# Optimization experiments

Measured on AMD Instinct MI355X. Metric: run time of the kernel, lower is better.

Reference implementation:

```python
import jax, jax.numpy as jnp
import numpy as np

N = 50000      # nodes
E = 800000     # edges (avg in-degree ~16)
IN = 64        # in_size
OUT = 64       # out_size
DELTA = 2.83   # PNA delta ~ log(avg_degree + 1)
MOM_EPS = 1e-30
BN_EPS = 1e-5


def setup_inputs() -> dict:
    key = jax.random.key(0)
    ks = jax.random.split(key, 8)
    node_feat = jax.random.normal(ks[0], (N, IN), dtype=jnp.float32)
    # Linear M: (2*IN -> IN); store weight as (2*IN, IN) for x @ W
    Wm = jax.random.normal(ks[1], (2 * IN, IN), dtype=jnp.float32) * (1.0 / np.sqrt(2 * IN))
    bm = jnp.zeros((IN,), jnp.float32)
    # Linear U: ((4 aggs * 3 scalers + 1) * IN -> OUT) = (13*IN -> OUT)
    Wu = jax.random.normal(ks[2], (13 * IN, OUT), dtype=jnp.float32) * (1.0 / np.sqrt(13 * IN))
    bu = jnp.zeros((OUT,), jnp.float32)
    gamma = jnp.ones((OUT,), jnp.float32)
    beta = jnp.zeros((OUT,), jnp.float32)
    src = jax.random.randint(ks[3], (E,), 0, N, dtype=jnp.int32)
    dst = jax.random.randint(ks[4], (E,), 0, N, dtype=jnp.int32)
    return {"node_feat": node_feat, "Wm": Wm, "bm": bm, "Wu": Wu, "bu": bu,
            "gamma": gamma, "beta": beta, "src": src, "dst": dst}


def _pna_forward(node_feat, Wm, bm, Wu, bu, gamma, beta, src, dst):
    # message MLP: M(h_src || h_dst) computed without materializing the concat
    msg = node_feat[src] @ Wm[:IN] + node_feat[dst] @ Wm[IN:] + bm  # (E, IN)

    deg = jax.ops.segment_sum(jnp.ones((E,), msg.dtype), dst, num_segments=N)  # (N,)
    safe_deg = jnp.maximum(deg, 1.0)[:, None]
    has_nbr = (deg > 0.0)[:, None]

    # multi-statistic ragged segment reduce
    s = jax.ops.segment_sum(msg, dst, num_segments=N)
    mean = s / safe_deg
    mean_sq = jax.ops.segment_sum(msg * msg, dst, num_segments=N) / safe_deg
    var = jax.nn.relu(mean_sq - mean * mean)
    std = jnp.sqrt(var + MOM_EPS)
    mx = jnp.where(has_nbr, jax.ops.segment_max(msg, dst, num_segments=N), 0.0)
    mn = jnp.where(has_nbr, jax.ops.segment_min(msg, dst, num_segments=N), 0.0)

    h = jnp.concatenate([mean, mx, mn, std], axis=1)  # (N, 4*IN)

    # scalers: identity, amplification log(D+1)/delta, attenuation delta/log(D+1)
    logD = jnp.log(deg + 1.0)[:, None]
    safe_logD = jnp.where(logD > 0.0, logD, 1.0)  # zero-degree rows masked below
    h_all = jnp.concatenate([h, h * (safe_logD / DELTA), h * (DELTA / safe_logD)], axis=1)
    h_neigh = jnp.where(has_nbr, h_all, 0.0)  # zero-degree nodes get 0 (DGL behavior)

    # update MLP + graph size norm (single graph: snorm = 1/sqrt(N))
    z = jnp.concatenate([node_feat, h_neigh], axis=1) @ Wu + bu  # (N, OUT)
    snorm = 1.0 / jnp.sqrt(jnp.asarray(N, z.dtype))
    z = z * snorm

    # BatchNorm1d, training mode (batch stats, biased variance)
    mu = jnp.mean(z, axis=0)
    v = jnp.mean((z - mu) ** 2, axis=0)
    return (z - mu) / jnp.sqrt(v + BN_EPS) * gamma + beta


def reference(node_feat, Wm, bm, Wu, bu, gamma, beta, src, dst):
    return _pna_forward(node_feat, Wm, bm, Wu, bu, gamma, beta, src, dst)
```

## Files before the change

### kernel.cpp

```cpp
#include <hip/hip_runtime.h>
#include <hip/hip_bf16.h>


#define DELTA_C 2.83f
#define BN_EPS_C 1e-5f
#define MOM_EPS_C 1e-30f
#define FLT_BIG 3.402823466e38f
#define BSHIFT 7
#define NBMAX 512

typedef __attribute__((ext_vector_type(8))) short bf16x8;
typedef __attribute__((ext_vector_type(4))) float f32x4;

static __device__ __forceinline__ unsigned short f2bf(float f) {
    unsigned u = __float_as_uint(f);
    unsigned r = (u + 0x7FFFu + ((u >> 16) & 1u)) >> 16;
    return (unsigned short)r;
}
static __device__ __forceinline__ unsigned pack2(float a, float b) {
    return (unsigned)f2bf(a) | ((unsigned)f2bf(b) << 16);
}
static __device__ __forceinline__ float bflo(unsigned u) { return __uint_as_float(u << 16); }
static __device__ __forceinline__ float bfhi(unsigned u) { return __uint_as_float(u & 0xFFFF0000u); }

__global__ __launch_bounds__(256) void repack_wu(
    const float* __restrict__ Wu, short* __restrict__ Wup,
    int* __restrict__ bcnt, int* __restrict__ gcur, float* __restrict__ bnacc)
{
    int t = threadIdx.x;
    if (blockIdx.x == 0) {
        bcnt[t] = 0; bcnt[t + 256] = 0;
        gcur[t] = 0; gcur[t + 256] = 0;
        if (t < 128) bnacc[t] = 0.f;
    }
    int idx = blockIdx.x * 256 + t;
    int lane = idx & 63, c = (idx >> 6) & 3, kc = idx >> 8;
    int kbase = kc * 32 + (lane >> 4) * 8;
    int col = c * 16 + (lane & 15);
    unsigned short o[8];
    #pragma unroll
    for (int i = 0; i < 8; ++i)
        o[i] = f2bf(Wu[(size_t)(kbase + i) * 64 + col]);
    uint4 u;
    u.x = o[0] | ((unsigned)o[1] << 16);
    u.y = o[2] | ((unsigned)o[3] << 16);
    u.z = o[4] | ((unsigned)o[5] << 16);
    u.w = o[6] | ((unsigned)o[7] << 16);
    *(uint4*)(Wup + (size_t)idx * 8) = u;
}

__global__ __launch_bounds__(256) void proj_ab(
    const float* __restrict__ x, const float* __restrict__ Wm,
    unsigned* __restrict__ Ab, float* __restrict__ B,
    unsigned* __restrict__ xbu, int n,
    const int* __restrict__ dst, int* __restrict__ bcnt, int e, int nb_chunk)
{
    __shared__ float wm[128][68];
    __shared__ float xs[64][68];
    __shared__ int h[NBMAX];
    int t = threadIdx.x;
    for (int i = t; i < 2048; i += 256) {
        int k = i >> 4, c4 = (i & 15) << 2;
        *(float4*)&wm[k][c4] = *(const float4*)&Wm[k * 64 + c4];
    }
    int row0 = blockIdx.x * 64;
    for (int i = t; i < 1024; i += 256) {
        int r = i >> 4, k4 = (i & 15) << 2;
        int row = row0 + r;
        float4 v = make_float4(0.f, 0.f, 0.f, 0.f);
        if (row < n) v = *(const float4*)&x[(size_t)row * 64 + k4];
        *(float4*)&xs[r][k4] = v;
    }
    __syncthreads();
    int tr = t >> 4, tc = t & 15, c0 = tc << 2;
    float a[4][4] = {}; float b[4][4] = {};
    #pragma unroll 8
    for (int k = 0; k < 64; ++k) {
        float4 wa = *(float4*)&wm[k][c0];
        float4 wb = *(float4*)&wm[64 + k][c0];
        #pragma unroll
        for (int i = 0; i < 4; ++i) {
            float xv = xs[tr * 4 + i][k];
            a[i][0] += xv * wa.x; a[i][1] += xv * wa.y; a[i][2] += xv * wa.z; a[i][3] += xv * wa.w;
            b[i][0] += xv * wb.x; b[i][1] += xv * wb.y; b[i][2] += xv * wb.z; b[i][3] += xv * wb.w;
        }
    }
    #pragma unroll
    for (int i = 0; i < 4; ++i) {
        int r = tr * 4 + i;
        int row = row0 + r;
        uint2 xp;
        xp.x = pack2(xs[r][c0], xs[r][c0 + 1]);
        xp.y = pack2(xs[r][c0 + 2], xs[r][c0 + 3]);
        *(uint2*)&xbu[(size_t)row * 32 + (c0 >> 1)] = xp;
        if (row < n) {
            uint2 ap;
            ap.x = pack2(a[i][0], a[i][1]);
            ap.y = pack2(a[i][2], a[i][3]);
            *(uint2*)&Ab[(size_t)row * 32 + (c0 >> 1)] = ap;
            *(float4*)&B[(size_t)row * 64 + c0] = make_float4(b[i][0], b[i][1], b[i][2], b[i][3]);
        }
    }
    if (blockIdx.x < nb_chunk) {
        __syncthreads();
        for (int bb = t; bb < NBMAX; bb += 256) h[bb] = 0;
        __syncthreads();
        int base = blockIdx.x * 4096;
        int cnt = min(4096, e - base);
        for (int i = t; i < cnt; i += 256)
            atomicAdd(&h[dst[base + i] >> BSHIFT], 1);
        __syncthreads();
        for (int bb = t; bb < NBMAX; bb += 256)
            if (h[bb]) atomicAdd(&bcnt[bb], h[bb]);
    }
}

__global__ __launch_bounds__(256) void bin_scatter(
    const int* __restrict__ src, const int* __restrict__ dst,
    const int* __restrict__ bcnt, int* __restrict__ gcur,
    unsigned* __restrict__ pairs_out, int e)
{
    __shared__ int hcnt[NBMAX], hstart[NBMAX], hcur[NBMAX], gpos[NBMAX], sgoff[NBMAX];
    __shared__ unsigned pairs[4096];
    int t = threadIdx.x;
    int base = blockIdx.x * 4096;
    int cnt = min(4096, e - base);
    for (int b = t; b < NBMAX; b += 256) hcnt[b] = 0;
    if (t < 64) {
        int v0 = bcnt[t * 8],     v1 = bcnt[t * 8 + 1], v2 = bcnt[t * 8 + 2], v3 = bcnt[t * 8 + 3];
        int v4 = bcnt[t * 8 + 4], v5 = bcnt[t * 8 + 5], v6 = bcnt[t * 8 + 6], v7 = bcnt[t * 8 + 7];
        int s = v0 + v1 + v2 + v3 + v4 + v5 + v6 + v7;
        int inc = s;
        #pragma unroll
        for (int st = 1; st < 64; st <<= 1) {
            int u = __shfl_up(inc, st);
            if (t >= st) inc += u;
        }
        int ex = inc - s;
        sgoff[t * 8] = ex;         ex += v0;
        sgoff[t * 8 + 1] = ex;     ex += v1;
        sgoff[t * 8 + 2] = ex;     ex += v2;
        sgoff[t * 8 + 3] = ex;     ex += v3;
        sgoff[t * 8 + 4] = ex;     ex += v4;
        sgoff[t * 8 + 5] = ex;     ex += v5;
        sgoff[t * 8 + 6] = ex;     ex += v6;
        sgoff[t * 8 + 7] = ex;
    }
    __syncthreads();

    int ls[16], ld[16];
    #pragma unroll
    for (int j = 0; j < 16; ++j) {
        int i = t + j * 256;
        ls[j] = 0; ld[j] = -1;
        if (i < cnt) {
            ls[j] = src[base + i];
            ld[j] = dst[base + i];
            atomicAdd(&hcnt[ld[j] >> BSHIFT], 1);
        }
    }
    __syncthreads();
    if (t < 64) {
        int v[8]; int s = 0;
        #pragma unroll
        for (int j = 0; j < 8; ++j) { v[j] = hcnt[t * 8 + j]; s += v[j]; }
        int inc = s;
        #pragma unroll
        for (int st = 1; st < 64; st <<= 1) {
            int u = __shfl_up(inc, st);
            if (t >= st) inc += u;
        }
        int ex = inc - s;
        #pragma unroll
        for (int j = 0; j < 8; ++j) {
            hstart[t * 8 + j] = ex;
            hcur[t * 8 + j] = ex;
            ex += v[j];
        }
    }
    __syncthreads();
    #pragma unroll
    for (int j = 0; j < 16; ++j) {
        if (ld[j] >= 0) {
            int pos = atomicAdd(&hcur[ld[j] >> BSHIFT], 1);
            pairs[pos] = ((unsigned)ls[j] << 16) | (unsigned)ld[j];
        }
    }
    __syncthreads();
    for (int b = t; b < NBMAX; b += 256) {
        int c = hcnt[b];
        if (c) gpos[b] = sgoff[b] + atomicAdd(&gcur[b], c);
    }
    __syncthreads();
    #pragma unroll
    for (int j = 0; j < 16; ++j) {
        int i = t + j * 256;
        if (i < cnt) {
            unsigned p = pairs[i];
            int b = (int)(p & 0xFFFFu) >> BSHIFT;
            pairs_out[gpos[b] + (i - hstart[b])] = p;
        }
    }
}

__global__ __launch_bounds__(128) void csr_fill(
    const unsigned* __restrict__ pairs, const int* __restrict__ bcnt,
    int* __restrict__ offs, int* __restrict__ csr, int n, int e)
{
    __shared__ int hist[128], pref[128], cur[128], sbase[1];
    int b = blockIdx.x, t = threadIdx.x;
    if (t < 64) {
        int acc = 0;
        for (int k = t; k < b; k += 64) acc += bcnt[k];
        acc += __shfl_down(acc, 32); acc += __shfl_down(acc, 16);
        acc += __shfl_down(acc, 8);  acc += __shfl_down(acc, 4);
        acc += __shfl_down(acc, 2);  acc += __shfl_down(acc, 1);
        if (t == 0) sbase[0] = acc;
    }
    hist[t] = 0;
    __syncthreads();
    int base = sbase[0], cnt = bcnt[b];
    int node0 = b << BSHIFT;
    for (int i = t; i < cnt; i += 128)
        atomicAdd(&hist[pairs[base + i] & 127u], 1);
    __syncthreads();
    if (t < 64) {
        int v0 = hist[2 * t], v1 = hist[2 * t + 1];
        int s = v0 + v1, inc = s;
        #pragma unroll
        for (int st = 1; st < 64; st <<= 1) {
            int u = __shfl_up(inc, st);
            if (t >= st) inc += u;
        }
        int ex = inc - s;
        pref[2 * t] = ex;       cur[2 * t] = ex;
        pref[2 * t + 1] = ex + v0; cur[2 * t + 1] = ex + v0;
    }
    __syncthreads();
    int node = node0 + t;
    if (node < n) offs[node] = base + pref[t];
    if (b == gridDim.x - 1 && t == 0) offs[n] = e;
    for (int i = t; i < cnt; i += 128) {
        unsigned p = pairs[base + i];
        int pos = atomicAdd(&cur[p & 127u], 1);
        csr[base + pos] = (int)(p >> 16);
    }
}

__global__ __launch_bounds__(256) void node_reduce(
    const unsigned* __restrict__ Ab, const float* __restrict__ Bp,
    const float* __restrict__ bm,
    const int* __restrict__ offs, const int* __restrict__ csr,
    unsigned* __restrict__ hbu, float* __restrict__ s1, float* __restrict__ s2,
    int n, int npad)
{
    int wid = threadIdx.x >> 6;
    int lane = threadIdx.x & 63;
    int node = blockIdx.x * 4 + wid;
    if (node >= npad) return;
    unsigned* hrow = hbu + (size_t)node * 128;
    int l32 = lane & 31;
    int half = lane >> 5;
    int beg = 0, dg = 0;
    if (node < n) { beg = offs[node]; dg = offs[node + 1] - beg; }
    if (dg == 0) {
        if (half == 0) {
            hrow[l32] = 0u; hrow[32 + l32] = 0u; hrow[64 + l32] = 0u; hrow[96 + l32] = 0u;
        }
        if (lane == 0) { s1[node] = 0.f; s2[node] = 0.f; }
        return;
    }

    float s0 = 0.f, s1a = 0.f, ss0 = 0.f, ss1 = 0.f;
    float mx0 = -FLT_BIG, mx1 = -FLT_BIG, mn0 = FLT_BIG, mn1 = FLT_BIG;

#define ACC(u) { float v0 = bflo(u), v1 = bfhi(u);                          \
    s0 += v0; s1a += v1;                                                    \
    ss0 = fmaf(v0, v0, ss0); ss1 = fmaf(v1, v1, ss1);                       \
    mx0 = fmaxf(mx0, v0); mx1 = fmaxf(mx1, v1);                             \
    mn0 = fminf(mn0, v0); mn1 = fminf(mn1, v1); }
#define GA(sel) Ab[(size_t)(sel) * 32 + l32]

    int j = beg, end = beg + dg;
    for (; j + 15 < end; j += 16) {
        int i0 = csr[j],      i1 = csr[j + 1],  i2 = csr[j + 2],  i3 = csr[j + 3];
        int i4 = csr[j + 4],  i5 = csr[j + 5],  i6 = csr[j + 6],  i7 = csr[j + 7];
        int i8 = csr[j + 8],  i9 = csr[j + 9],  i10 = csr[j + 10], i11 = csr[j + 11];
        int i12 = csr[j + 12], i13 = csr[j + 13], i14 = csr[j + 14], i15 = csr[j + 15];
        unsigned u0 = GA(half ? i1 : i0);
        unsigned u1 = GA(half ? i3 : i2);
        unsigned u2 = GA(half ? i5 : i4);
        unsigned u3 = GA(half ? i7 : i6);
        unsigned u4 = GA(half ? i9 : i8);
        unsigned u5 = GA(half ? i11 : i10);
        unsigned u6 = GA(half ? i13 : i12);
        unsigned u7 = GA(half ? i15 : i14);
        ACC(u0); ACC(u1); ACC(u2); ACC(u3);
        ACC(u4); ACC(u5); ACC(u6); ACC(u7);
    }
    for (; j + 7 < end; j += 8) {
        int i0 = csr[j],     i1 = csr[j + 1], i2 = csr[j + 2], i3 = csr[j + 3];
        int i4 = csr[j + 4], i5 = csr[j + 5], i6 = csr[j + 6], i7 = csr[j + 7];
        unsigned u0 = GA(half ? i1 : i0);
        unsigned u1 = GA(half ? i3 : i2);
        unsigned u2 = GA(half ? i5 : i4);
        unsigned u3 = GA(half ? i7 : i6);
        ACC(u0); ACC(u1); ACC(u2); ACC(u3);
    }
    for (; j + 1 < end; j += 2) {
        int i0 = csr[j], i1 = csr[j + 1];
        unsigned u0 = GA(half ? i1 : i0);
        ACC(u0);
    }
    if (j < end) {
        unsigned u0 = GA(csr[j]);
        if (half == 0) ACC(u0);
    }
#undef GA
#undef ACC

    s0 += __shfl_xor(s0, 32);  s1a += __shfl_xor(s1a, 32);
    ss0 += __shfl_xor(ss0, 32); ss1 += __shfl_xor(ss1, 32);
    mx0 = fmaxf(mx0, __shfl_xor(mx0, 32)); mx1 = fmaxf(mx1, __shfl_xor(mx1, 32));
    mn0 = fminf(mn0, __shfl_xor(mn0, 32)); mn1 = fminf(mn1, __shfl_xor(mn1, 32));

    float fd = (float)dg, inv = 1.0f / fd;
    float2 bv = *(const float2*)(Bp + (size_t)node * 64 + 2 * l32);
    float2 bmv = *(const float2*)(bm + 2 * l32);
    float bn0 = bv.x + bmv.x, bn1 = bv.y + bmv.y;
    float ma0 = s0 * inv, ma1 = s1a * inv;
    float var0 = ss0 * inv - ma0 * ma0; if (var0 < 0.f) var0 = 0.f;
    float var1 = ss1 * inv - ma1 * ma1; if (var1 < 0.f) var1 = 0.f;
    float sd0 = sqrtf(var0 + MOM_EPS_C), sd1 = sqrtf(var1 + MOM_EPS_C);

    if (half == 0) {
        hrow[l32]      = pack2(ma0 + bn0, ma1 + bn1);
        hrow[32 + l32] = pack2(mx0 + bn0, mx1 + bn1);
        hrow[64 + l32] = pack2(mn0 + bn0, mn1 + bn1);
        hrow[96 + l32] = pack2(sd0, sd1);
    }
    if (lane == 0) {
        float logD = logf(fd + 1.0f);
        s1[node] = logD / DELTA_C;
        s2[node] = DELTA_C / logD;
    }
}

__global__ __launch_bounds__(256) void gemm_mfma(
    const short* __restrict__ xb, const short* __restrict__ hb,
    const float* __restrict__ s1p, const float* __restrict__ s2p,
    const short* __restrict__ Wup, const float* __restrict__ bu,
    float* __restrict__ z, float* __restrict__ bnacc, int n, float snorm)
{
    __shared__ float bnl[4][2][64];
    int t = threadIdx.x;
    int lane = t & 63, w = t >> 6;
    int rb = blockIdx.x * 128 + w * 32;
    int r16 = lane & 15, kg = lane >> 4;

    f32x4 accx[2][4] = {};
    f32x4 acc1[2][4] = {};
    f32x4 acc2[2][4] = {};
    f32x4 acc3[2][4] = {};

    const short* xr0 = xb + (size_t)(rb + r16) * 64 + kg * 8;
    const short* xr1 = xr0 + 16 * 64;

    #pragma unroll
    for (int kc = 0; kc < 2; ++kc) {
        bf16x8 a0 = *(const bf16x8*)(xr0 + kc * 32);
        bf16x8 a1 = *(const bf16x8*)(xr1 + kc * 32);
        #pragma unroll
        for (int c = 0; c < 4; ++c) {
            bf16x8 b = *(const bf16x8*)(Wup + (size_t)((kc * 4 + c) * 64 + lane) * 8);
            accx[0][c] = __builtin_amdgcn_mfma_f32_16x16x32_bf16(a0, b, accx[0][c], 0, 0, 0);
            accx[1][c] = __builtin_amdgcn_mfma_f32_16x16x32_bf16(a1, b, accx[1][c], 0, 0, 0);
        }
    }

    const short* hr0 = hb + (size_t)(rb + r16) * 256 + kg * 8;
    const short* hr1 = hr0 + 16 * 256;

    #pragma unroll 1
    for (int kh = 0; kh < 8; ++kh) {
        bf16x8 a0 = *(const bf16x8*)(hr0 + kh * 32);
        bf16x8 a1 = *(const bf16x8*)(hr1 + kh * 32);
        #pragma unroll
        for (int c = 0; c < 4; ++c) {
            bf16x8 b1 = *(const bf16x8*)(Wup + (size_t)(((2  + kh) * 4 + c) * 64 + lane) * 8);
            bf16x8 b2 = *(const bf16x8*)(Wup + (size_t)(((10 + kh) * 4 + c) * 64 + lane) * 8);
            bf16x8 b3 = *(const bf16x8*)(Wup + (size_t)(((18 + kh) * 4 + c) * 64 + lane) * 8);
            acc1[0][c] = __builtin_amdgcn_mfma_f32_16x16x32_bf16(a0, b1, acc1[0][c], 0, 0, 0);
            acc1[1][c] = __builtin_amdgcn_mfma_f32_16x16x32_bf16(a1, b1, acc1[1][c], 0, 0, 0);
            acc2[0][c] = __builtin_amdgcn_mfma_f32_16x16x32_bf16(a0, b2, acc2[0][c], 0, 0, 0);
            acc2[1][c] = __builtin_amdgcn_mfma_f32_16x16x32_bf16(a1, b2, acc2[1][c], 0, 0, 0);
            acc3[0][c] = __builtin_amdgcn_mfma_f32_16x16x32_bf16(a0, b3, acc3[0][c], 0, 0, 0);
            acc3[1][c] = __builtin_amdgcn_mfma_f32_16x16x32_bf16(a1, b3, acc3[1][c], 0, 0, 0);
        }
    }

    float cs[4] = {}, css[4] = {};
    #pragma unroll
    for (int s = 0; s < 2; ++s) {
        int r0 = rb + s * 16 + kg * 4;
        float s1v[4], s2v[4];
        #pragma unroll
        for (int r = 0; r < 4; ++r) { s1v[r] = s1p[r0 + r]; s2v[r] = s2p[r0 + r]; }
        #pragma unroll
        for (int c = 0; c < 4; ++c) {
            int col = c * 16 + r16;
            float bval = bu[col];
            #pragma unroll
            for (int r = 0; r < 4; ++r) {
                int row = r0 + r;
                if (row < n) {
                    float v = (accx[s][c][r] + acc1[s][c][r]
                            + s1v[r] * acc2[s][c][r] + s2v[r] * acc3[s][c][r] + bval) * snorm;
                    z[(size_t)row * 64 + col] = v;
                    cs[c] += v;
                    css[c] = fmaf(v, v, css[c]);
                }
            }
        }
    }
    #pragma unroll
    for (int c = 0; c < 4; ++c) {
        float a = cs[c];  a += __shfl_xor(a, 16); a += __shfl_xor(a, 32); cs[c] = a;
        float b = css[c]; b += __shfl_xor(b, 16); b += __shfl_xor(b, 32); css[c] = b;
    }
    if (lane < 16) {
        #pragma unroll
        for (int c = 0; c < 4; ++c) {
            bnl[w][0][c * 16 + lane] = cs[c];
            bnl[w][1][c * 16 + lane] = css[c];
        }
    }
    __syncthreads();
    if (t < 128) {
        int st = t >> 6, cc = t & 63;
        float tot = bnl[0][st][cc] + bnl[1][st][cc] + bnl[2][st][cc] + bnl[3][st][cc];
        atomicAdd(&bnacc[st * 64 + cc], tot);
    }
}

__global__ __launch_bounds__(256) void bn_apply(
    float* __restrict__ z, const float* __restrict__ acc,
    const float* __restrict__ gamma, const float* __restrict__ beta, int n)
{
    float inv_n = 1.0f / (float)n;
    int tid = blockIdx.x * 256 + threadIdx.x;
    int c0 = (tid * 4) & 63;
    float sc[4], sh[4];
    #pragma unroll
    for (int k = 0; k < 4; ++k) {
        int c = c0 + k;
        float mu = acc[c] * inv_n;
        float var = acc[64 + c] * inv_n - mu * mu;
        if (var < 0.f) var = 0.f;
        float inv = rsqrtf(var + BN_EPS_C) * gamma[c];
        sc[k] = inv;
        sh[k] = beta[c] - mu * inv;
    }
    int total4 = n * 16;
    int stride = gridDim.x * 256;
    for (int i = tid; i < total4; i += stride) {
        float4 v = *(float4*)&z[(size_t)i * 4];
        v.x = fmaf(v.x, sc[0], sh[0]);
        v.y = fmaf(v.y, sc[1], sh[1]);
        v.z = fmaf(v.z, sc[2], sh[2]);
        v.w = fmaf(v.w, sc[3], sh[3]);
        *(float4*)&z[(size_t)i * 4] = v;
    }
}

extern "C" void kernel_launch(void* const* d_in, const int* in_sizes, int n_in,
                              void* d_out, int out_size, void* d_ws, size_t ws_size,
                              hipStream_t stream)
{
    const float* x     = (const float*)d_in[0];
    const float* Wm    = (const float*)d_in[1];
    const float* bm    = (const float*)d_in[2];
    const float* Wu    = (const float*)d_in[3];
    const float* bu    = (const float*)d_in[4];
    const float* gamma = (const float*)d_in[5];
    const float* beta  = (const float*)d_in[6];
    const int*   src   = (const int*)d_in[7];
    const int*   dst   = (const int*)d_in[8];

    int n = in_sizes[0] / 64;
    int e = in_sizes[7];
    int npad = ((n + 127) / 128) * 128;
    int nb = (n + 127) >> BSHIFT;
    float* z = (float*)d_out;

    char* w = (char*)d_ws;
    size_t off = 0;
    auto take = [&](size_t bytes) -> void* {
        void* p = w + off;
        off = (off + bytes + 255) & ~(size_t)255;
        return p;
    };
    unsigned* Ab    = (unsigned*)take((size_t)npad * 32 * sizeof(unsigned));
    float*    B     = (float*)take((size_t)n * 64 * sizeof(float));
    unsigned* xbu   = (unsigned*)take((size_t)npad * 32 * sizeof(unsigned));
    unsigned* hbu   = (unsigned*)take((size_t)npad * 128 * sizeof(unsigned));
    float*    s1    = (float*)take((size_t)npad * sizeof(float));
    float*    s2    = (float*)take((size_t)npad * sizeof(float));
    short*    Wup   = (short*)take((size_t)26 * 4 * 64 * 8 * sizeof(short));
    int*      offs  = (int*)take((size_t)(n + 1) * sizeof(int));
    int*      csr   = (int*)take((size_t)e * sizeof(int));
    unsigned* prs   = (unsigned*)take((size_t)e * sizeof(unsigned));
    int*      bcnt  = (int*)take((size_t)NBMAX * sizeof(int));
    int*      gcur  = (int*)take((size_t)NBMAX * sizeof(int));
    float*    bnacc = (float*)take(128 * sizeof(float));

    (void)n_in; (void)out_size; (void)ws_size;

    int nb_rows64 = npad / 64;
    int nb_chunk = (e + 4095) / 4096;

    repack_wu<<<26, 256, 0, stream>>>(Wu, Wup, bcnt, gcur, bnacc);
    proj_ab<<<nb_rows64, 256, 0, stream>>>(x, Wm, Ab, B, xbu, n, dst, bcnt, e, nb_chunk);
    bin_scatter<<<nb_chunk, 256, 0, stream>>>(src, dst, bcnt, gcur, prs, e);
    csr_fill<<<nb, 128, 0, stream>>>(prs, bcnt, offs, csr, n, e);
    node_reduce<<<(npad + 3) / 4, 256, 0, stream>>>(Ab, B, bm, offs, csr, hbu, s1, s2, n, npad);

    float snorm = (float)(1.0 / sqrt((double)n));
    gemm_mfma<<<npad / 128, 256, 0, stream>>>((const short*)xbu, (const short*)hbu,
                                              s1, s2, Wup, bu, z, bnacc, n, snorm);

    bn_apply<<<512, 256, 0, stream>>>(z, bnacc, gamma, beta, n);
}
```

Measured before the change: 120.5 us.

## Compute message projection with bf16 MFMA and fold weight repack into it

Replaces the fp32 FMA register-tile projection of node features by Wm with a bf16 MFMA GEMM over 128-row tiles. Wm is converted to bf16 MFMA fragments in shared memory. The separate Wu repack kernel is merged into the same launch, removing one kernel launch, and the dst histogram loop becomes grid-stride. The B half of the projection is now computed from bf16 inputs, which loses precision. Block 0 zeroes bcnt inside the same kernel where other blocks atomically add to it, which introduces an ordering race.

Result: faster. 109.3 us (-9.3%).

```diff
diff --git a/kernel.cpp b/kernel.cpp
--- a/kernel.cpp
+++ b/kernel.cpp
@@ -23,89 +23,130 @@
 static __device__ __forceinline__ float bflo(unsigned u) { return __uint_as_float(u << 16); }
 static __device__ __forceinline__ float bfhi(unsigned u) { return __uint_as_float(u & 0xFFFF0000u); }
 
-__global__ __launch_bounds__(256) void repack_wu(
+__global__ __launch_bounds__(256) void proj_mfma(
+    const float* __restrict__ x, const float* __restrict__ Wm,
+    unsigned* __restrict__ Ab, float* __restrict__ B,
+    unsigned* __restrict__ xbu, int n,
+    const int* __restrict__ dst, int* __restrict__ bcnt, int e, int nb_chunk,
     const float* __restrict__ Wu, short* __restrict__ Wup,
-    int* __restrict__ bcnt, int* __restrict__ gcur, float* __restrict__ bnacc)
-{
+    int* __restrict__ gcur, float* __restrict__ bnacc)
+{
+    __shared__ short xs[128][72];
+    __shared__ short wc[2][8][64][8];
+    __shared__ int h[NBMAX];
     int t = threadIdx.x;
+    int row0 = blockIdx.x * 128;
+
     if (blockIdx.x == 0) {
         bcnt[t] = 0; bcnt[t + 256] = 0;
         gcur[t] = 0; gcur[t + 256] = 0;
         if (t < 128) bnacc[t] = 0.f;
     }
-    int idx = blockIdx.x * 256 + t;
-    int lane = idx & 63, c = (idx >> 6) & 3, kc = idx >> 8;
-    int kbase = kc * 32 + (lane >> 4) * 8;
-    int col = c * 16 + (lane & 15);
-    unsigned short o[8];
-    #pragma unroll
-    for (int i = 0; i < 8; ++i)
-        o[i] = f2bf(Wu[(size_t)(kbase + i) * 64 + col]);
-    uint4 u;
-    u.x = o[0] | ((unsigned)o[1] << 16);
-    u.y = o[2] | ((unsigned)o[3] << 16);
-    u.z = o[4] | ((unsigned)o[5] << 16);
-    u.w = o[6] | ((unsigned)o[7] << 16);
-    *(uint4*)(Wup + (size_t)idx * 8) = u;
-}
-
-__global__ __launch_bounds__(256) void proj_ab(
-    const float* __restrict__ x, const float* __restrict__ Wm,
-    unsigned* __restrict__ Ab, float* __restrict__ B,
-    unsigned* __restrict__ xbu, int n,
-    const int* __restrict__ dst, int* __restrict__ bcnt, int e, int nb_chunk)
-{
-    __shared__ float wm[128][68];
-    __shared__ float xs[64][68];
-    __shared__ int h[NBMAX];
-    int t = threadIdx.x;
-    for (int i = t; i < 2048; i += 256) {
-        int k = i >> 4, c4 = (i & 15) << 2;
-        *(float4*)&wm[k][c4] = *(const float4*)&Wm[k * 64 + c4];
-    }
-    int row0 = blockIdx.x * 64;
-    for (int i = t; i < 1024; i += 256) {
-        int r = i >> 4, k4 = (i & 15) << 2;
+
+    if (blockIdx.x < 26) {
+        int idx = blockIdx.x * 256 + t;
+        int lane2 = idx & 63, c2 = (idx >> 6) & 3, kc2 = idx >> 8;
+        int kbase = kc2 * 32 + (lane2 >> 4) * 8;
+        int col = c2 * 16 + (lane2 & 15);
+        unsigned short o[8];
+        #pragma unroll
+        for (int i = 0; i < 8; ++i)
+            o[i] = f2bf(Wu[(size_t)(kbase + i) * 64 + col]);
+        uint4 u;
+        u.x = o[0] | ((unsigned)o[1] << 16);
+        u.y = o[2] | ((unsigned)o[3] << 16);
+        u.z = o[4] | ((unsigned)o[5] << 16);
+        u.w = o[6] | ((unsigned)o[7] << 16);
+        *(uint4*)(Wup + (size_t)idx * 8) = u;
+    }
+
+    for (int g = t; g < 1024; g += 256) {
+        int kc = g >> 9, c = (g >> 6) & 7, lane = g & 63;
+        int kb = kc * 32 + (lane >> 4) * 8;
+        int cc = c * 16 + (lane & 15);
+        const float* wsrc = (cc < 64) ? (Wm + (size_t)kb * 64 + cc)
+                                      : (Wm + (size_t)(64 + kb) * 64 + (cc - 64));
+        unsigned short o0 = f2bf(wsrc[0]);
+        unsigned short o1 = f2bf(wsrc[64]);
+        unsigned short o2 = f2bf(wsrc[128]);
+        unsigned short o3 = f2bf(wsrc[192]);
+        unsigned short o4 = f2bf(wsrc[256]);
+        unsigned short o5 = f2bf(wsrc[320]);
+        unsigned short o6 = f2bf(wsrc[384]);
+        unsigned short o7 = f2bf(wsrc[448]);
+        uint4 u;
+        u.x = o0 | ((unsigned)o1 << 16);
+        u.y = o2 | ((unsigned)o3 << 16);
+        u.z = o4 | ((unsigned)o5 << 16);
+        u.w = o6 | ((unsigned)o7 << 16);
+        *(uint4*)&wc[kc][c][lane][0] = u;
+    }
+
+    {
+        int r = t >> 1, hf = t & 1;
         int row = row0 + r;
-        float4 v = make_float4(0.f, 0.f, 0.f, 0.f);
-        if (row < n) v = *(const float4*)&x[(size_t)row * 64 + k4];
-        *(float4*)&xs[r][k4] = v;
-    }
-    __syncthreads();
-    int tr = t >> 4, tc = t & 15, c0 = tc << 2;
-    float a[4][4] = {}; float b[4][4] = {};
-    #pragma unroll 8
-    for (int k = 0; k < 64; ++k) {
-        float4 wa = *(float4*)&wm[k][c0];
-        float4 wb = *(float4*)&wm[64 + k][c0];
-        #pragma unroll
-        for (int i = 0; i < 4; ++i) {
-            float xv = xs[tr * 4 + i][k];
-            a[i][0] += xv * wa.x; a[i][1] += xv * wa.y; a[i][2] += xv * wa.z; a[i][3] += xv * wa.w;
-            b[i][0] += xv * wb.x; b[i][1] += xv * wb.y; b[i][2] += xv * wb.z; b[i][3] += xv * wb.w;
-        }
-    }
-    #pragma unroll
-    for (int i = 0; i < 4; ++i) {
-        int r = tr * 4 + i;
-        int row = row0 + r;
-        uint2 xp;
-        xp.x = pack2(xs[r][c0], xs[r][c0 + 1]);
-        xp.y = pack2(xs[r][c0 + 2], xs[r][c0 + 3]);
-        *(uint2*)&xbu[(size_t)row * 32 + (c0 >> 1)] = xp;
+        float4 f0 = {}, f1 = {}, f2 = {}, f3 = {}, f4 = {}, f5 = {}, f6 = {}, f7 = {};
         if (row < n) {
-            uint2 ap;
-            ap.x = pack2(a[i][0], a[i][1]);
-            ap.y = pack2(a[i][2], a[i][3]);
-            *(uint2*)&Ab[(size_t)row * 32 + (c0 >> 1)] = ap;
-            *(float4*)&B[(size_t)row * 64 + c0] = make_float4(b[i][0], b[i][1], b[i][2], b[i][3]);
-        }
-    }
-    if (blockIdx.x < nb_chunk) {
+            const float4* xr = (const float4*)(x + (size_t)row * 64 + hf * 32);
+            f0 = xr[0]; f1 = xr[1]; f2 = xr[2]; f3 = xr[3];
+            f4 = xr[4]; f5 = xr[5]; f6 = xr[6]; f7 = xr[7];
+        }
+        uint4 ua, ub, uc, ud;
+        ua.x = pack2(f0.x, f0.y); ua.y = pack2(f0.z, f0.w);
+        ua.z = pack2(f1.x, f1.y); ua.w = pack2(f1.z, f1.w);
+        ub.x = pack2(f2.x, f2.y); ub.y = pack2(f2.z, f2.w);
+        ub.z = pack2(f3.x, f3.y); ub.w = pack2(f3.z, f3.w);
+        uc.x = pack2(f4.x, f4.y); uc.y = pack2(f4.z, f4.w);
+        uc.z = pack2(f5.x, f5.y); uc.w = pack2(f5.z, f5.w);
+        ud.x = pack2(f6.x, f6.y); ud.y = pack2(f6.z, f6.w);
+        ud.z = pack2(f7.x, f7.y); ud.w = pack2(f7.z, f7.w);
+        uint4* xd = (uint4*)(xbu + (size_t)row * 32 + hf * 16);
+        xd[0] = ua; xd[1] = ub; xd[2] = uc; xd[3] = ud;
+        uint4* xl = (uint4*)&xs[r][hf * 32];
+        xl[0] = ua; xl[1] = ub; xl[2] = uc; xl[3] = ud;
+    }
+    __syncthreads();
+
+    int lane = t & 63, w = t >> 6;
+    int r16 = lane & 15, kg = lane >> 4;
+    int wr0 = w * 32;
+    f32x4 acc0[8] = {};
+    f32x4 acc1[8] = {};
+    #pragma unroll
+    for (int kc = 0; kc < 2; ++kc) {
+        bf16x8 a0 = *(const bf16x8*)&xs[wr0 + r16][kc * 32 + kg * 8];
+        bf16x8 a1 = *(const bf16x8*)&xs[wr0 + 16 + r16][kc * 32 + kg * 8];
+        #pragma unroll
+        for (int c = 0; c < 8; ++c) {
+            bf16x8 b = *(const bf16x8*)&wc[kc][c][lane][0];
+            acc0[c] = __builtin_amdgcn_mfma_f32_16x16x32_bf16(a0, b, acc0[c], 0, 0, 0);
+            acc1[c] = __builtin_amdgcn_mfma_f32_16x16x32_bf16(a1, b, acc1[c], 0, 0, 0);
+        }
+    }
+    short* AbS = (short*)Ab;
+    #pragma unroll
+    for (int c = 0; c < 8; ++c) {
+        #pragma unroll
+        for (int r = 0; r < 4; ++r) {
+            int rowA = row0 + wr0 + kg * 4 + r;
+            int rowB = rowA + 16;
+            if (c < 4) {
+                int col = c * 16 + r16;
+                if (rowA < n) AbS[(size_t)rowA * 64 + col] = (short)f2bf(acc0[c][r]);
+                if (rowB < n) AbS[(size_t)rowB * 64 + col] = (short)f2bf(acc1[c][r]);
+            } else {
+                int col = (c - 4) * 16 + r16;
+                if (rowA < n) B[(size_t)rowA * 64 + col] = acc0[c][r];
+                if (rowB < n) B[(size_t)rowB * 64 + col] = acc1[c][r];
+            }
+        }
+    }
+
+    for (int ch = blockIdx.x; ch < nb_chunk; ch += gridDim.x) {
         __syncthreads();
         for (int bb = t; bb < NBMAX; bb += 256) h[bb] = 0;
         __syncthreads();
-        int base = blockIdx.x * 4096;
+        int base = ch * 4096;
         int cnt = min(4096, e - base);
         for (int i = t; i < cnt; i += 256)
             atomicAdd(&h[dst[base + i] >> BSHIFT], 1);
@@ -516,11 +557,11 @@
 
     (void)n_in; (void)out_size; (void)ws_size;
 
-    int nb_rows64 = npad / 64;
     int nb_chunk = (e + 4095) / 4096;
 
-    repack_wu<<<26, 256, 0, stream>>>(Wu, Wup, bcnt, gcur, bnacc);
-    proj_ab<<<nb_rows64, 256, 0, stream>>>(x, Wm, Ab, B, xbu, n, dst, bcnt, e, nb_chunk);
+    proj_mfma<<<npad / 128, 256, 0, stream>>>(x, Wm, Ab, B, xbu, n,
+                                              dst, bcnt, e, nb_chunk,
+                                              Wu, Wup, gcur, bnacc);
     bin_scatter<<<nb_chunk, 256, 0, stream>>>(src, dst, bcnt, gcur, prs, e);
     csr_fill<<<nb, 128, 0, stream>>>(prs, bcnt, offs, csr, n, e);
     node_reduce<<<(npad + 3) / 4, 256, 0, stream>>>(Ab, B, bm, offs, csr, hbu, s1, s2, n, npad);
```
